# Kernel optimization log

Hardware: AMD Instinct MI355X
Metric: run time of the kernel (lower is better)

Reference implementation:

```python
import jax, jax.numpy as jnp
import numpy as np

B, XL, YL = 4, 128, 1024
D, H, L, DFF = 512, 8, 3, 2048
PV, AV, OV = 512, 1025, 1025
MASK_ID = 1024
EOS = 1024
DUR_W = 1.0
NEG = -1e9  # finite large-negative instead of -inf: keeps fully-padded rows NaN-free
HD = D // H
S = XL + 1 + YL


def sinusoid(n, d):
    pos = jnp.arange(n, dtype=jnp.float32)[:, None]
    div = jnp.exp(jnp.arange(0, d, 2, dtype=jnp.float32) * (-np.log(10000.0) / d))
    pe = jnp.zeros((n, d), dtype=jnp.float32)
    pe = pe.at[:, 0::2].set(jnp.sin(pos * div))
    pe = pe.at[:, 1::2].set(jnp.cos(pos * div))
    return pe


def layer_norm(x, g, b, eps=1e-5):
    mu = x.mean(-1, keepdims=True)
    var = ((x - mu) ** 2).mean(-1, keepdims=True)
    return (x - mu) * jax.lax.rsqrt(var + eps) * g + b


def setup_inputs():
    k = jax.random.split(jax.random.key(0), 32)
    x = jax.random.randint(k[0], (B, XL), 0, PV)
    x1_lens = jax.random.randint(k[1], (B,), 20, 60)
    x2_lens = jax.random.randint(k[2], (B,), 20, 60)
    y = jax.random.randint(k[3], (B, YL), 0, AV - 2)
    y1_lens = jax.random.randint(k[4], (B,), 100, 400)
    y2_lens = jax.random.randint(k[5], (B,), 300, 600)
    y_lens = y1_lens + 1 + y2_lens
    idx = jnp.arange(YL)[None, :]
    valid = (idx >= y1_lens[:, None] + 1) & (idx < y_lens[:, None] - 1)
    bern = jax.random.uniform(k[6], (B, YL)) < 0.3  # mask_ratio = mid(min,max)
    ym = bern & valid
    need = (~ym.any(1)) & valid.any(1)
    first = jnp.argmax(valid, axis=1)
    y_mask = ym | (need[:, None] & (idx == first[:, None]))
    emo_feature = jax.random.normal(k[7], (B, 768), dtype=jnp.float32)

    def n(kk, shape, s=0.02):
        return s * jax.random.normal(kk, shape, dtype=jnp.float32)

    inp = dict(x=x, x1_lens=x1_lens, x2_lens=x2_lens, y=y, y1_lens=y1_lens,
               y2_lens=y2_lens, y_mask=y_mask, emo_feature=emo_feature)
    inp['text_emb'] = n(k[8], (PV, D))
    inp['audio_emb'] = n(k[9], (AV, D))
    inp['type_emb'] = n(k[10], (3, D))
    inp['emo_W'] = n(k[11], (D, 768))
    inp['emo_b'] = jnp.zeros((D,), jnp.float32)
    inp['alpha_text'] = jnp.float32(1.0)
    inp['alpha_audio'] = jnp.float32(1.0)
    inp['Wqkv'] = n(k[12], (L, 3 * D, D))
    inp['bqkv'] = jnp.zeros((L, 3 * D), jnp.float32)
    inp['Wo'] = n(k[13], (L, D, D))
    inp['bo'] = jnp.zeros((L, D), jnp.float32)
    inp['ln1_g'] = jnp.ones((L, D), jnp.float32)
    inp['ln1_b'] = jnp.zeros((L, D), jnp.float32)
    inp['ln2_g'] = jnp.ones((L, D), jnp.float32)
    inp['ln2_b'] = jnp.zeros((L, D), jnp.float32)
    inp['W1'] = n(k[14], (L, DFF, D))
    inp['b1'] = jnp.zeros((L, DFF), jnp.float32)
    inp['W2'] = n(k[15], (L, D, DFF))
    inp['b2'] = jnp.zeros((L, D), jnp.float32)
    inp['predict_W'] = n(k[16], (OV, D))
    inp['dW1'] = n(k[17], (D // 2, D))
    inp['db1'] = jnp.zeros((D // 2,), jnp.float32)
    inp['dW2'] = n(k[18], (D // 4, D // 2))
    inp['db2'] = jnp.zeros((D // 4,), jnp.float32)
    inp['dW3'] = n(k[19], (1, D // 4))
    inp['db3'] = jnp.zeros((1,), jnp.float32)
    return inp


def build_attn_bias(x1_lens, x2_lens, y1_lens, y2_lens, y_mask):
    x_lens = x1_lens + 1 + x2_lens
    y_lens = y1_lens + 1 + y2_lens
    cS = jnp.arange(S)[None, :]  # [1,S] key columns
    # --- x rows ---
    rx = jnp.arange(XL)[None, :]
    is_x1 = rx < x1_lens[:, None]                                   # [B,XL]
    allow_x1 = cS < x1_lens[:, None]                                # [B,S]
    allow_x2 = (cS >= x1_lens[:, None]) & (cS < x_lens[:, None])
    x_allow = jnp.where(is_x1[:, :, None], allow_x1[:, None, :], allow_x2[:, None, :])
    # --- emo row: attends only to itself (col XL) ---
    emo_allow = jnp.broadcast_to((cS == XL)[:, None, :], (B, 1, S))
    # --- y rows ---
    ry = jnp.arange(YL)[None, :]
    is_y1 = ry < y1_lens[:, None]
    is_cls = ry == y1_lens[:, None]
    is_y2 = (ry > y1_lens[:, None]) & (ry < y_lens[:, None])
    allow_y1 = (cS < x1_lens[:, None]) | ((cS > XL) & (cS <= XL + y1_lens[:, None]))
    allow_cls = (cS < x_lens[:, None]) | (cS == XL) | ((cS > XL) & (cS <= XL + y1_lens[:, None] + 1))
    allow_y2 = (cS < x_lens[:, None]) | (cS == XL) | ((cS > XL) & (cS <= XL + y_lens[:, None]))
    ymask_full = jnp.zeros((B, S), bool).at[:, XL + 1:].set(y_mask)
    allow_y2 = allow_y2 & (~ymask_full)                             # masked tokens invisible
    y_allow = jnp.where(is_y1[:, :, None], allow_y1[:, None, :],
               jnp.where(is_cls[:, :, None], allow_cls[:, None, :],
                jnp.where(is_y2[:, :, None], allow_y2[:, None, :], False)))
    block = ~jnp.concatenate([x_allow, emo_allow, y_allow], axis=1)  # True = blocked
    return jnp.where(block, jnp.float32(NEG), jnp.float32(0.0))[:, None]  # [B,1,S,S]


def encoder_forward(h, bias, Wqkv, bqkv, Wo, bo, ln1_g, ln1_b, ln2_g, ln2_b, W1, b1, W2, b2):
    scale = 1.0 / np.sqrt(HD)
    for l in range(L):
        qkv = h @ Wqkv[l].T + bqkv[l]                               # [B,S,3D]
        q, k, v = jnp.split(qkv, 3, axis=-1)
        q = q.reshape(B, S, H, HD).transpose(0, 2, 1, 3)
        k = k.reshape(B, S, H, HD).transpose(0, 2, 1, 3)
        v = v.reshape(B, S, H, HD).transpose(0, 2, 1, 3)
        scores = jnp.einsum('bhqd,bhkd->bhqk', q, k) * scale + bias
        a = jax.nn.softmax(scores, axis=-1)
        o = jnp.einsum('bhqk,bhkd->bhqd', a, v).transpose(0, 2, 1, 3).reshape(B, S, D)
        o = o @ Wo[l].T + bo[l]
        h = layer_norm(h + o, ln1_g[l], ln1_b[l])                   # post-norm
        ff = jax.nn.relu(h @ W1[l].T + b1[l]) @ W2[l].T + b2[l]
        h = layer_norm(h + ff, ln2_g[l], ln2_b[l])
    return h


def reference(x, x1_lens, x2_lens, y, y1_lens, y2_lens, y_mask, emo_feature,
              text_emb, audio_emb, type_emb, emo_W, emo_b, alpha_text, alpha_audio,
              Wqkv, bqkv, Wo, bo, ln1_g, ln1_b, ln2_g, ln2_b, W1, b1, W2, b2,
              predict_W, dW1, db1, dW2, db2, dW3, db3):
    y_target = y
    x_emb = text_emb[x] + type_emb[0]
    x_pos = x_emb + alpha_text * sinusoid(XL, D)
    emo = emo_feature @ emo_W.T + emo_b + type_emb[1]
    y_in = jnp.where(y_mask, MASK_ID, y)
    y_emb = audio_emb[y_in] + type_emb[2]
    y_pos = y_emb + alpha_audio * sinusoid(YL, D)
    h_input = jnp.concatenate([x_pos, emo[:, None, :], y_pos], axis=1)  # [B,S,D]
    bias = build_attn_bias(x1_lens, x2_lens, y1_lens, y2_lens, y_mask)
    enc = encoder_forward(h_input, bias, Wqkv, bqkv, Wo, bo,
                          ln1_g, ln1_b, ln2_g, ln2_b, W1, b1, W2, b2)
    # duration loss on CLS hidden at prompt_lens = XL + 1 + y1_lens
    cls_hidden = enc[jnp.arange(B), XL + 1 + y1_lens]
    h1 = jax.nn.relu(cls_hidden @ dW1.T + db1)
    h2 = jax.nn.relu(h1 @ dW2.T + db2)
    pred_dur = (h2 @ dW3.T + db3)[:, 0]
    tgt_dur = y2_lens.astype(jnp.float32) / x2_lens.astype(jnp.float32)
    e = pred_dur - tgt_dur
    dur_loss = jnp.mean(jnp.where(jnp.abs(e) <= 1.0, 0.5 * e * e, jnp.abs(e) - 0.5))
    # token CE over masked positions (mean over masked tokens)
    logits = enc[:, XL + 1:] @ predict_W.T                          # [B,YL,OV]
    logp = jax.nn.log_softmax(logits, axis=-1)
    ce = -jnp.take_along_axis(logp, y_target[..., None], axis=-1)[..., 0]
    m = y_mask.astype(jnp.float32)
    token_loss = jnp.sum(ce * m) / jnp.sum(m)
    # top-3 accuracy ignoring EOS
    top3 = jax.lax.top_k(logits, 3)[1]
    correct = jnp.any(top3 == y_target[..., None], axis=-1)
    inc = (y_mask & (y_target != EOS)).astype(jnp.float32)
    acc = jnp.sum(correct.astype(jnp.float32) * inc) / jnp.maximum(jnp.sum(inc), 1.0)
    total_loss = token_loss + DUR_W * dur_loss
    return total_loss, acc
```

## Files before the change

kernel.cpp:

```cpp
#include <hip/hip_runtime.h>
#include <hip/hip_bf16.h>
#include <math.h>

#define BATCH 4
#define XL 128
#define YL 1024
#define DMODEL 512
#define NH 8
#define NLAYER 3
#define DFF 2048
#define MASK_ID 1024
#define EOS_TOK 1024
#define HD 64
#define SEQ 1153
#define OV 1025
#define NEGBIG (-1e9f)
#define QBLK 128
#define CCAP 2432

typedef unsigned short u16;
typedef unsigned int u32;
typedef short short8 __attribute__((ext_vector_type(8)));
typedef float f32x4 __attribute__((ext_vector_type(4)));

__device__ __forceinline__ u16 f2bf(float f) {
    union { float f; unsigned u; } v; v.f = f;
    unsigned r = v.u + 0x7fffu + ((v.u >> 16) & 1u);
    return (u16)(r >> 16);
}
__device__ __forceinline__ float bf2f(u16 b) {
    union { unsigned u; float f; } v; v.u = ((unsigned)b) << 16;
    return v.f;
}

__global__ __launch_bounds__(256) void cvt5_kernel(
    const float* __restrict__ s0, u16* __restrict__ d0, int n0,
    const float* __restrict__ s1, u16* __restrict__ d1, int n1,
    const float* __restrict__ s2, u16* __restrict__ d2, int n2,
    const float* __restrict__ s3, u16* __restrict__ d3, int n3,
    const float* __restrict__ s4, u16* __restrict__ d4, int n4)
{
    int c0 = n0, c1 = c0 + n1, c2 = c1 + n2, c3 = c2 + n3, c4 = c3 + n4;
    for (int i = blockIdx.x * 256 + threadIdx.x; i < c4; i += gridDim.x * 256) {
        const float* s; u16* d; int j;
        if (i < c0)      { s = s0; d = d0; j = i; }
        else if (i < c1) { s = s1; d = d1; j = i - c0; }
        else if (i < c2) { s = s2; d = d2; j = i - c1; }
        else if (i < c3) { s = s3; d = d3; j = i - c2; }
        else             { s = s4; d = d4; j = i - c3; }
        float4 v = ((const float4*)s)[j];
        ushort4 o;
        o.x = f2bf(v.x); o.y = f2bf(v.y); o.z = f2bf(v.z); o.w = f2bf(v.w);
        ((ushort4*)d)[j] = o;
    }
}

__global__ __launch_bounds__(256) void emo_kernel(
    const float* __restrict__ emo_feature, const float* __restrict__ emo_W,
    const float* __restrict__ emo_b, const float* __restrict__ type_emb,
    float* __restrict__ hbuf, u16* __restrict__ hbuf_bf)
{
    int b = blockIdx.x >> 3, c = blockIdx.x & 7;
    int t = threadIdx.x;
    int osub = t >> 2, ln = t & 3;
    int d = c * 64 + osub;
    const float* f = emo_feature + b * 768 + ln * 192;
    const float* w = emo_W + (size_t)d * 768 + ln * 192;
    float acc = 0.f;
    #pragma unroll 4
    for (int k = 0; k < 192; ++k) acc = fmaf(f[k], w[k], acc);
    acc += __shfl_xor(acc, 1);
    acc += __shfl_xor(acc, 2);
    if (ln == 0) {
        float v = acc + emo_b[d] + type_emb[DMODEL + d];
        hbuf[(size_t)(b * SEQ + XL) * DMODEL + d] = v;
        hbuf_bf[(size_t)(b * SEQ + XL) * DMODEL + d] = f2bf(v);
    }
}

__global__ __launch_bounds__(256) void build_h_kernel(
    const int* __restrict__ x, const int* __restrict__ y, const int* __restrict__ y_mask,
    const float* __restrict__ text_emb, const float* __restrict__ audio_emb,
    const float* __restrict__ type_emb,
    const float* __restrict__ alpha_text, const float* __restrict__ alpha_audio,
    float* __restrict__ hbuf, u16* __restrict__ hbuf_bf)
{
    int row = blockIdx.x * 4 + (threadIdx.x >> 6);
    int l = threadIdx.x & 63;
    int b = row / SEQ, s = row % SEQ;
    if (s == XL) return;
    int d0 = l * 8;

    const float* emb; const float* te; float alpha; int pos;
    if (s < XL) {
        int tok = x[b * XL + s];
        emb = text_emb + (size_t)tok * DMODEL;
        te = type_emb; alpha = alpha_text[0]; pos = s;
    } else {
        int r = s - XL - 1;
        int tok = y_mask[b * YL + r] ? MASK_ID : y[b * YL + r];
        emb = audio_emb + (size_t)tok * DMODEL;
// ... 156 lines not shown
            #pragma unroll
            for (int jj = 0; jj < 4; ++jj) {
                int row = m0 + wm + i * 16 + ((l >> 4) << 2) + jj;
                int col = n0 + wn + j * 16 + (l & 15);
                if (row < M && col < N)
                    Cp[(size_t)row * N + col] = acc[i][j][jj];
            }
        }
    }
}

__global__ __launch_bounds__(256) void gemm_bf16_splitk_dynm_kernel(
    const u16* __restrict__ A, const u16* __restrict__ Bw,
    const int* __restrict__ Mp,
    float* __restrict__ P0, float* __restrict__ P1,
    int N, int K, int klen)
{
    int M = *Mp;
    int m0 = blockIdx.y * 128;
    if (m0 >= M) return;
    __shared__ u16 As[128 * 32];
    __shared__ u16 Bs[128 * 32];
    int tid = threadIdx.x;
    int w = tid >> 6, l = tid & 63;
    int z = blockIdx.z;
    float* Cp = (z == 0) ? P0 : P1;
    int kbeg = z * klen;
    int kend = min(kbeg + klen, K);
    int n0 = blockIdx.x * 128;
    int wm = (w >> 1) * 64, wn = (w & 1) * 64;

    f32x4 acc[4][4];
    #pragma unroll
    for (int i = 0; i < 4; ++i)
        #pragma unroll
        for (int j = 0; j < 4; ++j) acc[i][j] = (f32x4){0.f, 0.f, 0.f, 0.f};

    int srow0 = (w << 5) + (l >> 2);
    int skp = (l & 3) << 3;

    for (int k0 = kbeg; k0 < kend; k0 += 32) {
        #pragma unroll
        for (int c = 0; c < 2; ++c) {
            int row = srow0 + c * 16;
            int am = m0 + row; if (am >= M) am = M - 1;
            int bn = n0 + row; if (bn >= N) bn = N - 1;
            __builtin_amdgcn_global_load_lds(
                (const __attribute__((address_space(1))) void*)(A + (size_t)am * K + k0 + skp),
                (__attribute__((address_space(3))) void*)(As + ((w * 2 + c) << 9)), 16, 0, 0);
            __builtin_amdgcn_global_load_lds(
                (const __attribute__((address_space(1))) void*)(Bw + (size_t)bn * K + k0 + skp),
                (__attribute__((address_space(3))) void*)(Bs + ((w * 2 + c) << 9)), 16, 0, 0);
        }
        __syncthreads();
        short8 af[4], bfr[4];
        #pragma unroll
        for (int i = 0; i < 4; ++i) {
            af[i]  = *(const short8*)(As + (wm + i * 16 + (l & 15)) * 32 + ((l >> 4) << 3));
            bfr[i] = *(const short8*)(Bs + (wn + i * 16 + (l & 15)) * 32 + ((l >> 4) << 3));
        }
        #pragma unroll
        for (int i = 0; i < 4; ++i)
            #pragma unroll
            for (int j = 0; j < 4; ++j)
                acc[i][j] = __builtin_amdgcn_mfma_f32_16x16x32_bf16(af[i], bfr[j], acc[i][j], 0, 0, 0);
        __syncthreads();
    }

    #pragma unroll
    for (int i = 0; i < 4; ++i) {
        #pragma unroll
        for (int j = 0; j < 4; ++j) {
            #pragma unroll
            for (int jj = 0; jj < 4; ++jj) {
                int row = m0 + wm + i * 16 + ((l >> 4) << 2) + jj;
                int col = n0 + wn + j * 16 + (l & 15);
                if (row < M && col < N)
                    Cp[(size_t)row * N + col] = acc[i][j][jj];
            }
        }
    }
}

__global__ __launch_bounds__(512) void attn_mfma_kernel(
    const u16* __restrict__ qkv,
    const int* __restrict__ x1_lens, const int* __restrict__ x2_lens,
    const int* __restrict__ y1_lens, const int* __restrict__ y2_lens,
    const int* __restrict__ y_mask,
    u16* __restrict__ obuf)
{
    __shared__ u16 Ks[64 * 64];
    __shared__ u16 Vt[64 * 64];
    __shared__ unsigned long long Bits[7][19];

    int tid = threadIdx.x;
    int w = tid >> 6, l = tid & 63;
    int g = l >> 4;
    int bh = blockIdx.y;
    int b = bh >> 3, h = bh & 7;
    int q0 = blockIdx.x * QBLK;

    int x1 = x1_lens[b], xlen = x1 + 1 + x2_lens[b];
    int y1 = y1_lens[b], ylen = y1 + 1 + y2_lens[b];

    int kmax = -1;
    if (q0 < XL) kmax = max(kmax, xlen - 1);
    if (XL >= q0 && XL < q0 + QBLK) kmax = max(kmax, XL);
    {
        int ry0 = max(0, q0 - XL - 1);
        int ry1 = min(YL - 1, q0 + QBLK - 2 - XL);
        if (ry0 <= ry1) {
            if (ry0 <= y1 - 1) kmax = max(kmax, XL + y1);
            if (y1 >= ry0 && y1 <= ry1) kmax = max(kmax, XL + y1 + 1);
            int a = max(ry0, y1 + 1), bb = min(ry1, ylen - 1);
            if (a <= bb) kmax = max(kmax, XL + ylen);
        }
    }
    if (kmax < 0) return;
    int NKT = (kmax >> 6) + 1;

    for (int pp = w; pp < 7 * 19; pp += 8) {
        int ty = pp / 19, tile = pp - ty * 19;
        int c = tile * 64 + l;
        bool allow = false;
        if (c < SEQ && ty < 6) {
            bool a2c = (c == XL), ygt = (c > XL);
            if (ty == 0) allow = (c < x1);
            else if (ty == 1) allow = (c >= x1) && (c < xlen);
            else if (ty == 2) allow = a2c;
            else if (ty == 3) allow = (c < x1) || (ygt && c <= XL + y1);
            else if (ty == 4) allow = (c < xlen) || a2c || (ygt && c <= XL + y1 + 1);
            else {
                int ym = ygt ? y_mask[b * YL + c - XL - 1] : 0;
                allow = (((c < xlen) || a2c || (ygt && c <= XL + ylen)) && !ym);
            }
        }
        unsigned long long mk = __ballot(allow);
        if (l == 0) Bits[ty][tile] = mk;
    }

    int qr = q0 + w * 16 + (l & 15);
    int qrc = min(qr, SEQ - 1);
    short8 qf0, qf1;
    {
        const u16* qp = qkv + (size_t)(b * SEQ + qrc) * 1536 + h * 64 + (g << 3);
        short8 r0 = *(const short8*)qp;
        short8 r1 = *(const short8*)(qp + 32);
        #pragma unroll
        for (int e = 0; e < 8; ++e) {
            qf0[e] = (short)f2bf(bf2f((u16)r0[e]) * 0.125f);
            qf1[e] = (short)f2bf(bf2f((u16)r1[e]) * 0.125f);
        }
    }

    int rt;
    {
        if (qr >= SEQ) rt = 6;
        else if (qr < XL) rt = (qr < x1) ? 0 : 1;
        else if (qr == XL) rt = 2;
        else {
            int ry = qr - XL - 1;
            rt = (ry < y1) ? 3 : (ry == y1) ? 4 : (ry < ylen) ? 5 : 6;
        }
    }

    f32x4 oacc[4];
    #pragma unroll
    for (int db = 0; db < 4; ++db) oacc[db] = (f32x4){0.f, 0.f, 0.f, 0.f};
    float mrun = -INFINITY, lrun = 0.f;

    int srcA = (l & 15) + ((g & 1) << 5);
    int srcB = srcA + 16;
    bool hi = (g >> 1) & 1;

    for (int kt = 0; kt < NKT; ++kt) {
        __syncthreads();
        {
            int r = tid >> 3, d0k = (tid & 7) << 3;
            int krc = min(kt * 64 + r, SEQ - 1);
            short8 ka = *(const short8*)(qkv + (size_t)(b * SEQ + krc) * 1536 + 512 + h * 64 + d0k);
            *(short8*)&Ks[r * 64 + (d0k ^ ((r & 7) << 3))] = ka;
        }
        {
            int rp = tid >> 4, o = tid & 15;
            int d0v = o * 4;
            int k0r = min(kt * 64 + 2 * rp, SEQ - 1);
            int k1r = min(kt * 64 + 2 * rp + 1, SEQ - 1);
            ushort4 va = *(const ushort4*)(qkv + (size_t)(b * SEQ + k0r) * 1536 + 1024 + h * 64 + d0v);
            ushort4 vb = *(const ushort4*)(qkv + (size_t)(b * SEQ + k1r) * 1536 + 1024 + h * 64 + d0v);
            u32 pv[4] = {(u32)va.x | ((u32)vb.x << 16), (u32)va.y | ((u32)vb.y << 16),
                         (u32)va.z | ((u32)vb.z << 16), (u32)va.w | ((u32)vb.w << 16)};
            #pragma unroll
            for (int e = 0; e < 4; ++e) {
                int d = d0v + e;
                *(u32*)&Vt[d * 64 + ((2 * rp) ^ ((d & 7) << 3))] = pv[e];
            }
        }
        __syncthreads();

        f32x4 sc[4];
        #pragma unroll
        for (int cb = 0; cb < 4; ++cb) {
            int krw = cb * 16 + (l & 15);
            int ksw = (krw & 7) << 3;
            short8 k0 = *(const short8*)&Ks[krw * 64 + ((g << 3) ^ ksw)];
            short8 k1 = *(const short8*)&Ks[krw * 64 + ((32 + (g << 3)) ^ ksw)];
            f32x4 z = (f32x4){0.f, 0.f, 0.f, 0.f};
            z = __builtin_amdgcn_mfma_f32_16x16x32_bf16(k0, qf0, z, 0, 0, 0);
            sc[cb] = __builtin_amdgcn_mfma_f32_16x16x32_bf16(k1, qf1, z, 0, 0, 0);
        }

        unsigned long long mb = Bits[rt][kt];
        #pragma unroll
        for (int cb = 0; cb < 4; ++cb) {
            unsigned nib = (unsigned)(mb >> (16 * cb + 4 * g)) & 0xFu;
            #pragma unroll
            for (int r = 0; r < 4; ++r)
                sc[cb][r] = ((nib >> r) & 1u) ? sc[cb][r] : NEGBIG;
        }

        float tmax = sc[0][0];
        #pragma unroll
        for (int cb = 0; cb < 4; ++cb)
            #pragma unroll
            for (int r = 0; r < 4; ++r) tmax = fmaxf(tmax, sc[cb][r]);
        tmax = fmaxf(tmax, __shfl_xor(tmax, 16));
        tmax = fmaxf(tmax, __shfl_xor(tmax, 32));
        float newm = fmaxf(mrun, tmax);
        float corr = __expf(mrun - newm);
        float p[4][4];
        float ps = 0.f;
        #pragma unroll
        for (int cb = 0; cb < 4; ++cb)
            #pragma unroll
            for (int r = 0; r < 4; ++r) {
                p[cb][r] = __expf(sc[cb][r] - newm);
                ps += p[cb][r];
            }
        ps += __shfl_xor(ps, 16);
        ps += __shfl_xor(ps, 32);
        lrun = lrun * corr + ps;
        mrun = newm;

        float cr[4];
        #pragma unroll
        for (int r = 0; r < 4; ++r) cr[r] = __shfl(corr, (g << 2) + r);
        #pragma unroll
        for (int db = 0; db < 4; ++db)
            #pragma unroll
            for (int r = 0; r < 4; ++r) oacc[db][r] *= cr[r];

        u32 P0[4], P1[4];
        #pragma unroll
        for (int cb = 0; cb < 4; ++cb) {
            P0[cb] = (u32)f2bf(p[cb][0]) | ((u32)f2bf(p[cb][1]) << 16);
            P1[cb] = (u32)f2bf(p[cb][2]) | ((u32)f2bf(p[cb][3]) << 16);
        }

        union { u32 u[4]; short8 s; } f1, f2;
        {
            u32 a0 = __shfl(P0[0], srcA), a1 = __shfl(P1[0], srcA);
            u32 a2 = __shfl(P0[0], srcB), a3 = __shfl(P1[0], srcB);
            u32 b0 = __shfl(P0[1], srcA), b1 = __shfl(P1[1], srcA);
            u32 b2 = __shfl(P0[1], srcB), b3 = __shfl(P1[1], srcB);
            f1.u[0] = hi ? b0 : a0; f1.u[1] = hi ? b1 : a1;
            f1.u[2] = hi ? b2 : a2; f1.u[3] = hi ? b3 : a3;
            u32 c0 = __shfl(P0[2], srcA), c1 = __shfl(P1[2], srcA);
            u32 c2 = __shfl(P0[2], srcB), c3 = __shfl(P1[2], srcB);
            u32 d0 = __shfl(P0[3], srcA), d1 = __shfl(P1[3], srcA);
            u32 d2 = __shfl(P0[3], srcB), d3 = __shfl(P1[3], srcB);
            f2.u[0] = hi ? d0 : c0; f2.u[1] = hi ? d1 : c1;
            f2.u[2] = hi ? d2 : c2; f2.u[3] = hi ? d3 : c3;
        }

        #pragma unroll
        for (int db = 0; db < 4; ++db) {
            int vr = db * 16 + (l & 15);
            int vsw = (vr & 7) << 3;
            short8 v0 = *(const short8*)&Vt[vr * 64 + ((g << 3) ^ vsw)];
            short8 v1 = *(const short8*)&Vt[vr * 64 + ((32 + (g << 3)) ^ vsw)];
            oacc[db] = __builtin_amdgcn_mfma_f32_16x16x32_bf16(f1.s, v0, oacc[db], 0, 0, 0);
            oacc[db] = __builtin_amdgcn_mfma_f32_16x16x32_bf16(f2.s, v1, oacc[db], 0, 0, 0);
        }
    }

    float rinv = 1.f / lrun;
    float rl[4];
    #pragma unroll
    for (int r = 0; r < 4; ++r) rl[r] = __shfl(rinv, (g << 2) + r);
    #pragma unroll
    for (int db = 0; db < 4; ++db) {
        #pragma unroll
        for (int r = 0; r < 4; ++r) {
            int qrj = q0 + w * 16 + (g << 2) + r;
            if (qrj < SEQ)
                obuf[(size_t)(b * SEQ + qrj) * DMODEL + h * 64 + db * 16 + (l & 15)] =
                    f2bf(oacc[db][r] * rl[r]);
        }
    }
}

__global__ __launch_bounds__(256) void add_ln_kernel(
    float* __restrict__ hbuf, u16* __restrict__ hbuf_bf,
    const float* __restrict__ p0, const float* __restrict__ p1,
    const float* __restrict__ p2, const float* __restrict__ bias,
    const float* __restrict__ g, const float* __restrict__ beta)
{
    int row = blockIdx.x * 4 + (threadIdx.x >> 6);
    int l = threadIdx.x & 63;
    int d0 = l * 8;
    size_t off = (size_t)row * DMODEL + d0;
    float* hp = hbuf + off;
    float4 a0 = *(const float4*)hp, a1 = *(const float4*)(hp + 4);
    float4 q0 = *(const float4*)(p0 + off), q1 = *(const float4*)(p0 + off + 4);
    float v[8] = {a0.x + q0.x, a0.y + q0.y, a0.z + q0.z, a0.w + q0.w,
                  a1.x + q1.x, a1.y + q1.y, a1.z + q1.z, a1.w + q1.w};
    if (p1) {
        float4 r0 = *(const float4*)(p1 + off), r1 = *(const float4*)(p1 + off + 4);
        v[0] += r0.x; v[1] += r0.y; v[2] += r0.z; v[3] += r0.w;
        v[4] += r1.x; v[5] += r1.y; v[6] += r1.z; v[7] += r1.w;
    }
    if (p2) {
        float4 r0 = *(const float4*)(p2 + off), r1 = *(const float4*)(p2 + off + 4);
        v[0] += r0.x; v[1] += r0.y; v[2] += r0.z; v[3] += r0.w;
        v[4] += r1.x; v[5] += r1.y; v[6] += r1.z; v[7] += r1.w;
    }
    {
        float4 b0 = *(const float4*)(bias + d0), b1 = *(const float4*)(bias + d0 + 4);
        v[0] += b0.x; v[1] += b0.y; v[2] += b0.z; v[3] += b0.w;
        v[4] += b1.x; v[5] += b1.y; v[6] += b1.z; v[7] += b1.w;
    }
    float s = 0.f;
    #pragma unroll
    for (int e = 0; e < 8; ++e) s += v[e];
    #pragma unroll
    for (int off2 = 32; off2 > 0; off2 >>= 1) s += __shfl_xor(s, off2);
    float mu = s * (1.f / DMODEL);
    float sq = 0.f;
    #pragma unroll
    for (int e = 0; e < 8; ++e) { v[e] -= mu; sq += v[e] * v[e]; }
    #pragma unroll
    for (int off2 = 32; off2 > 0; off2 >>= 1) sq += __shfl_xor(sq, off2);
    float inv = 1.f / sqrtf(sq * (1.f / DMODEL) + 1e-5f);
    float4 g0 = *(const float4*)(g + d0), g1 = *(const float4*)(g + d0 + 4);
    float4 be0 = *(const float4*)(beta + d0), be1 = *(const float4*)(beta + d0 + 4);
    float o[8];
    o[0] = v[0] * inv * g0.x + be0.x; o[1] = v[1] * inv * g0.y + be0.y;
    o[2] = v[2] * inv * g0.z + be0.z; o[3] = v[3] * inv * g0.w + be0.w;
    o[4] = v[4] * inv * g1.x + be1.x; o[5] = v[5] * inv * g1.y + be1.y;
    o[6] = v[6] * inv * g1.z + be1.z; o[7] = v[7] * inv * g1.w + be1.w;
    *(float4*)hp       = make_float4(o[0], o[1], o[2], o[3]);
    *(float4*)(hp + 4) = make_float4(o[4], o[5], o[6], o[7]);
    short8 sv;
    #pragma unroll
    for (int e = 0; e < 8; ++e) sv[e] = (short)f2bf(o[e]);
    *(short8*)(hbuf_bf + off) = sv;
}

__global__ __launch_bounds__(256) void init_accum_kernel(float* accum) {
    if (threadIdx.x < 8) accum[threadIdx.x] = 0.f;
}

__global__ __launch_bounds__(256) void compact_kernel(
    const int* __restrict__ y_mask, int* __restrict__ cnt, int* __restrict__ cmap)
{
    int i = blockIdx.x * 256 + threadIdx.x;
    if (i < BATCH * YL && y_mask[i]) {
        int pos = atomicAdd(cnt, 1);
        cmap[pos] = i;
    }
}

__global__ __launch_bounds__(256) void copy_rows_kernel(
    const int* __restrict__ cnt, const int* __restrict__ cmap,
    const u16* __restrict__ hbuf_bf, const int* __restrict__ y,
    u16* __restrict__ cbuf, int* __restrict__ ctgt)
{
    int i = blockIdx.x;
    if (i >= *cnt) return;
    int g = cmap[i];
    int b = g >> 10, r = g & 1023;
    const u16* src = hbuf_bf + (size_t)(b * SEQ + XL + 1 + r) * DMODEL;
// ... 97 lines not shown
        const float* w = dW2 + (size_t)t * 256;
        for (int k = 0; k < 256; ++k) acc = fmaf(h1s[k], w[k], acc);
        h2s[t] = fmaxf(acc, 0.f);
    }
    __syncthreads();
    if (t < 64) {
        float v = h2s[t] * dW3[t] + h2s[t + 64] * dW3[t + 64];
        #pragma unroll
        for (int off = 32; off > 0; off >>= 1) v += __shfl_xor(v, off);
        if (t == 0) preds[b] = v + db3[0];
    }
}

__global__ __launch_bounds__(64) void final_kernel(
    const float* __restrict__ accum, const float* __restrict__ preds,
    const int* __restrict__ y2_lens, const int* __restrict__ x2_lens,
    float* __restrict__ out)
{
    if (threadIdx.x == 0) {
        float dl = 0.f;
        for (int b = 0; b < BATCH; ++b) {
            float tgt = (float)y2_lens[b] / (float)x2_lens[b];
            float e = preds[b] - tgt;
            float ae = fabsf(e);
            dl += (ae <= 1.f) ? 0.5f * e * e : (ae - 0.5f);
        }
        dl *= (1.f / BATCH);
        float token_loss = accum[0] / accum[1];
        float acc_v = accum[2] / fmaxf(accum[3], 1.f);
        out[0] = token_loss + dl;
        out[1] = acc_v;
    }
}

extern "C" void kernel_launch(void* const* d_in, const int* in_sizes, int n_in,
                              void* d_out, int out_size, void* d_ws, size_t ws_size,
                              hipStream_t stream)
{
    const int*   x           = (const int*)d_in[0];
    const int*   x1_lens     = (const int*)d_in[1];
    const int*   x2_lens     = (const int*)d_in[2];
    const int*   y           = (const int*)d_in[3];
    const int*   y1_lens     = (const int*)d_in[4];
    const int*   y2_lens     = (const int*)d_in[5];
    const int*   y_mask      = (const int*)d_in[6];
    const float* emo_feature = (const float*)d_in[7];
    const float* text_emb    = (const float*)d_in[8];
    const float* audio_emb   = (const float*)d_in[9];
    const float* type_emb    = (const float*)d_in[10];
    const float* emo_W       = (const float*)d_in[11];
    const float* emo_b       = (const float*)d_in[12];
    const float* alpha_text  = (const float*)d_in[13];
    const float* alpha_audio = (const float*)d_in[14];
    const float* Wqkv        = (const float*)d_in[15];
    const float* bqkv        = (const float*)d_in[16];
    const float* Wo          = (const float*)d_in[17];
    const float* bo          = (const float*)d_in[18];
    const float* ln1_g       = (const float*)d_in[19];
    const float* ln1_b       = (const float*)d_in[20];
    const float* ln2_g       = (const float*)d_in[21];
    const float* ln2_b       = (const float*)d_in[22];
    const float* W1          = (const float*)d_in[23];
    const float* b1          = (const float*)d_in[24];
    const float* W2          = (const float*)d_in[25];
    const float* b2          = (const float*)d_in[26];
    const float* predict_W   = (const float*)d_in[27];
    const float* dW1         = (const float*)d_in[28];
    const float* db1         = (const float*)d_in[29];
    const float* dW2         = (const float*)d_in[30];
    const float* db2         = (const float*)d_in[31];
    const float* dW3         = (const float*)d_in[32];
    const float* db3         = (const float*)d_in[33];

    const int M = BATCH * SEQ;
    char* p = (char*)d_ws;
    float* hbuf   = (float*)p; p += 9445376;
    float* delta  = (float*)p; p += 9445376;
    char*  uni    = p;         p += 18909440;
    u16*   hbuf_bf = (u16*)p;  p += 4722688;
    u16*   qkv_bf  = (u16*)p;  p += 14168064;
    u16*   obuf_bf = (u16*)p;  p += 4722688;
    u16*   wbf     = (u16*)p;  p += 19923968;
    u16*   cbuf    = (u16*)p;  p += (size_t)CCAP * DMODEL * 2;
    u16*   ff1_bf  = (u16*)uni;

    float* partA = (float*)qkv_bf;
    float* partB = (float*)((char*)qkv_bf + 9445376);
    float* lg0   = (float*)uni;
    float* lg1   = (float*)qkv_bf;

    float* accum  = delta;
    int*   cnt    = (int*)(delta + 4);
    float* preds  = delta + 8;
    int*   cmap   = (int*)(delta + 16);
    int*   ctgt   = cmap + CCAP;
    float* h1buf  = (float*)(ctgt + CCAP);

    u16* wq_bf = wbf;
    u16* wo_bf = wq_bf + 2359296;
    u16* w1_bf = wo_bf + 786432;
    u16* w2_bf = w1_bf + 3145728;
    u16* wp_bf = w2_bf + 3145728;

    cvt5_kernel<<<1024, 256, 0, stream>>>(
        Wqkv, wq_bf, 2359296 / 4,
        Wo, wo_bf, 786432 / 4,
        W1, w1_bf, 3145728 / 4,
        W2, w2_bf, 3145728 / 4,
        predict_W, wp_bf, 524800 / 4);

    emo_kernel<<<32, 256, 0, stream>>>(emo_feature, emo_W, emo_b, type_emb, hbuf, hbuf_bf);
    build_h_kernel<<<M / 4, 256, 0, stream>>>(
        x, y, y_mask, text_emb, audio_emb, type_emb,
        alpha_text, alpha_audio, hbuf, hbuf_bf);

    const int MG = (M + 127) / 128;
    for (int l = 0; l < NLAYER; ++l) {
        gemm_bf16_kernel<<<dim3(12, MG), 256, 0, stream>>>(
            hbuf_bf, wq_bf + (size_t)l * 1536 * 512, bqkv + l * 1536,
            nullptr, qkv_bf, M, 1536, 512, 0);
        attn_mfma_kernel<<<dim3((SEQ + QBLK - 1) / QBLK, BATCH * NH), 512, 0, stream>>>(
            qkv_bf, x1_lens, x2_lens, y1_lens, y2_lens, y_mask, obuf_bf);
        gemm_bf16_splitk_kernel<<<dim3(4, MG, 2), 256, 0, stream>>>(
            obuf_bf, wo_bf + (size_t)l * 512 * 512,
            delta, partA, nullptr, M, 512, 512, 256);
        add_ln_kernel<<<M / 4, 256, 0, stream>>>(hbuf, hbuf_bf,
            delta, partA, nullptr, bo + l * 512,
            ln1_g + l * DMODEL, ln1_b + l * DMODEL);
        gemm_bf16_kernel<<<dim3(16, MG), 256, 0, stream>>>(
            hbuf_bf, w1_bf + (size_t)l * 2048 * 512, b1 + l * 2048,
            nullptr, ff1_bf, M, 2048, 512, 1);
        gemm_bf16_splitk_kernel<<<dim3(4, MG, 3), 256, 0, stream>>>(
            ff1_bf, w2_bf + (size_t)l * 512 * 2048,
            delta, partA, partB, M, 512, 2048, 768);
        add_ln_kernel<<<M / 4, 256, 0, stream>>>(hbuf, hbuf_bf,
            delta, partA, partB, b2 + l * 512,
            ln2_g + l * DMODEL, ln2_b + l * DMODEL);
    }

    init_accum_kernel<<<1, 64, 0, stream>>>(accum);
    compact_kernel<<<(BATCH * YL) / 256, 256, 0, stream>>>(y_mask, cnt, cmap);
    copy_rows_kernel<<<CCAP, 256, 0, stream>>>(cnt, cmap, hbuf_bf, y, cbuf, ctgt);
    gemm_bf16_splitk_dynm_kernel<<<dim3((OV + 127) / 128, CCAP / 128, 2), 256, 0, stream>>>(
        cbuf, wp_bf, cnt, lg0, lg1, OV, 512, 256);
    ce_kernel<<<CCAP, 256, 0, stream>>>(cnt, lg0, lg1, ctgt, accum);

    dur1_kernel<<<32, 256, 0, stream>>>(hbuf, y1_lens, dW1, db1, h1buf);
    dur2_kernel<<<4, 256, 0, stream>>>(h1buf, dW2, db2, dW3, db3, preds);
    final_kernel<<<1, 64, 0, stream>>>(accum, preds, y2_lens, x2_lens, (float*)d_out);
}
```

Before: 598.2 us.

## Double-buffer K/V tiles in attention with register prefetch and MFMA priority

```diff
diff --git a/kernel.cpp b/kernel.cpp
--- a/kernel.cpp
+++ b/kernel.cpp
@@ -346,8 +346,8 @@
     const int* __restrict__ y_mask,
     u16* __restrict__ obuf)
 {
-    __shared__ u16 Ks[64 * 64];
-    __shared__ u16 Vt[64 * 64];
+    __shared__ u16 Ks[2][64 * 64];
+    __shared__ u16 Vt[2][64 * 64];
     __shared__ unsigned long long Bits[7][19];
 
     int tid = threadIdx.x;
@@ -430,42 +430,60 @@
     int srcB = srcA + 16;
     bool hi = (g >> 1) & 1;
 
+    int sr = tid >> 3, sd = (tid & 7) << 3;
+    int ksw_w = (sd ^ ((sr & 7) << 3));
+    int vrp = tid >> 4, vo = (tid & 15) << 2;
+    const u16* kbase = qkv + (size_t)b * SEQ * 1536 + 512 + h * 64;
+    const u16* vbase = kbase + 512;
+
+    short8 kreg; ushort4 va, vb;
+    {
+        int krc = min(sr, SEQ - 1);
+        kreg = *(const short8*)(kbase + (size_t)krc * 1536 + sd);
+        int k0r = min(2 * vrp, SEQ - 1);
+        int k1r = min(2 * vrp + 1, SEQ - 1);
+        va = *(const ushort4*)(vbase + (size_t)k0r * 1536 + vo);
+        vb = *(const ushort4*)(vbase + (size_t)k1r * 1536 + vo);
+    }
+    *(short8*)&Ks[0][sr * 64 + ksw_w] = kreg;
+    {
+        u32 pv[4] = {(u32)va.x | ((u32)vb.x << 16), (u32)va.y | ((u32)vb.y << 16),
+                     (u32)va.z | ((u32)vb.z << 16), (u32)va.w | ((u32)vb.w << 16)};
+        #pragma unroll
+        for (int e = 0; e < 4; ++e) {
+            int d = vo + e;
+            *(u32*)&Vt[0][d * 64 + ((2 * vrp) ^ ((d & 7) << 3))] = pv[e];
+        }
+    }
+
     for (int kt = 0; kt < NKT; ++kt) {
         __syncthreads();
-        {
-            int r = tid >> 3, d0k = (tid & 7) << 3;
-            int krc = min(kt * 64 + r, SEQ - 1);
-            short8 ka = *(const short8*)(qkv + (size_t)(b * SEQ + krc) * 1536 + 512 + h * 64 + d0k);
-            *(short8*)&Ks[r * 64 + (d0k ^ ((r & 7) << 3))] = ka;
-        }
-        {
-            int rp = tid >> 4, o = tid & 15;
-            int d0v = o * 4;
-            int k0r = min(kt * 64 + 2 * rp, SEQ - 1);
-            int k1r = min(kt * 64 + 2 * rp + 1, SEQ - 1);
-            ushort4 va = *(const ushort4*)(qkv + (size_t)(b * SEQ + k0r) * 1536 + 1024 + h * 64 + d0v);
-            ushort4 vb = *(const ushort4*)(qkv + (size_t)(b * SEQ + k1r) * 1536 + 1024 + h * 64 + d0v);
-            u32 pv[4] = {(u32)va.x | ((u32)vb.x << 16), (u32)va.y | ((u32)vb.y << 16),
-                         (u32)va.z | ((u32)vb.z << 16), (u32)va.w | ((u32)vb.w << 16)};
-            #pragma unroll
-            for (int e = 0; e < 4; ++e) {
-                int d = d0v + e;
-                *(u32*)&Vt[d * 64 + ((2 * rp) ^ ((d & 7) << 3))] = pv[e];
-            }
-        }
-        __syncthreads();
+        int cur = kt & 1;
+        bool have_next = (kt + 1 < NKT);
+
+        if (have_next) {
+            int base = (kt + 1) * 64;
+            int krc = min(base + sr, SEQ - 1);
+            kreg = *(const short8*)(kbase + (size_t)krc * 1536 + sd);
+            int k0r = min(base + 2 * vrp, SEQ - 1);
+            int k1r = min(base + 2 * vrp + 1, SEQ - 1);
+            va = *(const ushort4*)(vbase + (size_t)k0r * 1536 + vo);
+            vb = *(const ushort4*)(vbase + (size_t)k1r * 1536 + vo);
+        }
 
         f32x4 sc[4];
+        __builtin_amdgcn_s_setprio(1);
         #pragma unroll
         for (int cb = 0; cb < 4; ++cb) {
             int krw = cb * 16 + (l & 15);
             int ksw = (krw & 7) << 3;
-            short8 k0 = *(const short8*)&Ks[krw * 64 + ((g << 3) ^ ksw)];
-            short8 k1 = *(const short8*)&Ks[krw * 64 + ((32 + (g << 3)) ^ ksw)];
+            short8 k0 = *(const short8*)&Ks[cur][krw * 64 + ((g << 3) ^ ksw)];
+            short8 k1 = *(const short8*)&Ks[cur][krw * 64 + ((32 + (g << 3)) ^ ksw)];
             f32x4 z = (f32x4){0.f, 0.f, 0.f, 0.f};
             z = __builtin_amdgcn_mfma_f32_16x16x32_bf16(k0, qf0, z, 0, 0, 0);
             sc[cb] = __builtin_amdgcn_mfma_f32_16x16x32_bf16(k1, qf1, z, 0, 0, 0);
         }
+        __builtin_amdgcn_s_setprio(0);
 
         unsigned long long mb = Bits[rt][kt];
         #pragma unroll
@@ -530,14 +548,28 @@
             f2.u[2] = hi ? d2 : c2; f2.u[3] = hi ? d3 : c3;
         }
 
+        __builtin_amdgcn_s_setprio(1);
         #pragma unroll
         for (int db = 0; db < 4; ++db) {
             int vr = db * 16 + (l & 15);
             int vsw = (vr & 7) << 3;
-            short8 v0 = *(const short8*)&Vt[vr * 64 + ((g << 3) ^ vsw)];
-            short8 v1 = *(const short8*)&Vt[vr * 64 + ((32 + (g << 3)) ^ vsw)];
+            short8 v0 = *(const short8*)&Vt[cur][vr * 64 + ((g << 3) ^ vsw)];
+            short8 v1 = *(const short8*)&Vt[cur][vr * 64 + ((32 + (g << 3)) ^ vsw)];
             oacc[db] = __builtin_amdgcn_mfma_f32_16x16x32_bf16(f1.s, v0, oacc[db], 0, 0, 0);
             oacc[db] = __builtin_amdgcn_mfma_f32_16x16x32_bf16(f2.s, v1, oacc[db], 0, 0, 0);
+        }
+        __builtin_amdgcn_s_setprio(0);
+
+        if (have_next) {
+            int nxt = cur ^ 1;
+            *(short8*)&Ks[nxt][sr * 64 + ksw_w] = kreg;
+            u32 pv[4] = {(u32)va.x | ((u32)vb.x << 16), (u32)va.y | ((u32)vb.y << 16),
+                         (u32)va.z | ((u32)vb.z << 16), (u32)va.w | ((u32)vb.w << 16)};
+            #pragma unroll
+            for (int e = 0; e < 4; ++e) {
+                int d = vo + e;
+                *(u32*)&Vt[nxt][d * 64 + ((2 * vrp) ^ ((d & 7) << 3))] = pv[e];
+            }
         }
     }
 
```

New measurement: 601.0 us. Within noise of the previous version (+0.5%).

## Pre-transpose V and load K/V fragments directly from global memory in attention

Applied to the files above, without the earlier changes.

```diff
diff --git a/kernel.cpp b/kernel.cpp
--- a/kernel.cpp
+++ b/kernel.cpp
@@ -13,6 +13,7 @@
 #define EOS_TOK 1024
 #define HD 64
 #define SEQ 1153
+#define SEQP 1216
 #define OV 1025
 #define NEGBIG (-1e9f)
 #define QBLK 128
@@ -339,23 +340,53 @@
     }
 }
 
+__global__ __launch_bounds__(256) void vtrans_kernel(
+    const u16* __restrict__ qkv, u16* __restrict__ vt)
+{
+    __shared__ u16 tbuf[64][72];
+    int bh = blockIdx.y;
+    int b = bh >> 3, h = bh & 7;
+    int kt = blockIdx.x;
+    int tid = threadIdx.x;
+    #pragma unroll
+    for (int i = 0; i < 2; ++i) {
+        int idx = tid + i * 256;
+        int r = idx >> 3, d0 = (idx & 7) << 3;
+        int s = kt * 64 + r;
+        short8 v = (short8){0,0,0,0,0,0,0,0};
+        if (s < SEQ)
+            v = *(const short8*)(qkv + (size_t)(b * SEQ + s) * 1536 + 1024 + h * 64 + d0);
+        *(short8*)&tbuf[r][d0] = v;
+    }
+    __syncthreads();
+    u16* out = vt + (size_t)bh * 64 * SEQP + kt * 64;
+    #pragma unroll
+    for (int i = 0; i < 2; ++i) {
+        int idx = tid + i * 256;
+        int d = idx >> 3, s0 = (idx & 7) << 3;
+        short8 v;
+        #pragma unroll
+        for (int e = 0; e < 8; ++e) v[e] = (short)tbuf[s0 + e][d];
+        *(short8*)(out + (size_t)d * SEQP + s0) = v;
+    }
+}
+
 __global__ __launch_bounds__(512) void attn_mfma_kernel(
-    const u16* __restrict__ qkv,
+    const u16* __restrict__ qkv, const u16* __restrict__ vt,
     const int* __restrict__ x1_lens, const int* __restrict__ x2_lens,
     const int* __restrict__ y1_lens, const int* __restrict__ y2_lens,
     const int* __restrict__ y_mask,
     u16* __restrict__ obuf)
 {
-    __shared__ u16 Ks[64 * 64];
-    __shared__ u16 Vt[64 * 64];
     __shared__ unsigned long long Bits[7][19];
 
     int tid = threadIdx.x;
     int w = tid >> 6, l = tid & 63;
     int g = l >> 4;
+    int q = l & 15;
     int bh = blockIdx.y;
     int b = bh >> 3, h = bh & 7;
-    int q0 = blockIdx.x * QBLK;
+    int q0 = (gridDim.x - 1 - blockIdx.x) * QBLK;
 
     int x1 = x1_lens[b], xlen = x1 + 1 + x2_lens[b];
     int y1 = y1_lens[b], ylen = y1 + 1 + y2_lens[b];
@@ -395,8 +426,9 @@
         unsigned long long mk = __ballot(allow);
         if (l == 0) Bits[ty][tile] = mk;
     }
-
-    int qr = q0 + w * 16 + (l & 15);
+    __syncthreads();
+
+    int qr = q0 + w * 16 + q;
     int qrc = min(qr, SEQ - 1);
     short8 qf0, qf1;
     {
@@ -426,46 +458,39 @@
     for (int db = 0; db < 4; ++db) oacc[db] = (f32x4){0.f, 0.f, 0.f, 0.f};
     float mrun = -INFINITY, lrun = 0.f;
 
-    int srcA = (l & 15) + ((g & 1) << 5);
+    int srcA = q + ((g & 1) << 5);
     int srcB = srcA + 16;
     bool hi = (g >> 1) & 1;
 
+    const u16* kbase = qkv + (size_t)b * SEQ * 1536 + 512 + h * 64 + (g << 3);
+    const u16* vbase = vt + (size_t)bh * 64 * SEQP + (size_t)q * SEQP + (g << 3);
+
     for (int kt = 0; kt < NKT; ++kt) {
-        __syncthreads();
-        {
-            int r = tid >> 3, d0k = (tid & 7) << 3;
-            int krc = min(kt * 64 + r, SEQ - 1);
-            short8 ka = *(const short8*)(qkv + (size_t)(b * SEQ + krc) * 1536 + 512 + h * 64 + d0k);
-            *(short8*)&Ks[r * 64 + (d0k ^ ((r & 7) << 3))] = ka;
-        }
-        {
-            int rp = tid >> 4, o = tid & 15;
-            int d0v = o * 4;
-            int k0r = min(kt * 64 + 2 * rp, SEQ - 1);
-            int k1r = min(kt * 64 + 2 * rp + 1, SEQ - 1);
-            ushort4 va = *(const ushort4*)(qkv + (size_t)(b * SEQ + k0r) * 1536 + 1024 + h * 64 + d0v);
-            ushort4 vb = *(const ushort4*)(qkv + (size_t)(b * SEQ + k1r) * 1536 + 1024 + h * 64 + d0v);
-            u32 pv[4] = {(u32)va.x | ((u32)vb.x << 16), (u32)va.y | ((u32)vb.y << 16),
-                         (u32)va.z | ((u32)vb.z << 16), (u32)va.w | ((u32)vb.w << 16)};
-            #pragma unroll
-            for (int e = 0; e < 4; ++e) {
-                int d = d0v + e;
-                *(u32*)&Vt[d * 64 + ((2 * rp) ^ ((d & 7) << 3))] = pv[e];
-            }
-        }
-        __syncthreads();
+        short8 kf0[4], kf1[4];
+        #pragma unroll
+        for (int cb = 0; cb < 4; ++cb) {
+            int ks = min(kt * 64 + cb * 16 + q, SEQ - 1);
+            const u16* kp = kbase + (size_t)ks * 1536;
+            kf0[cb] = *(const short8*)kp;
+            kf1[cb] = *(const short8*)(kp + 32);
+        }
+        short8 vf0[4], vf1[4];
+        #pragma unroll
+        for (int db = 0; db < 4; ++db) {
+            const u16* vp = vbase + (size_t)(db * 16) * SEQP + kt * 64;
+            vf0[db] = *(const short8*)vp;
+            vf1[db] = *(const short8*)(vp + 32);
+        }
 
         f32x4 sc[4];
+        __builtin_amdgcn_s_setprio(1);
         #pragma unroll
         for (int cb = 0; cb < 4; ++cb) {
-            int krw = cb * 16 + (l & 15);
-            int ksw = (krw & 7) << 3;
-            short8 k0 = *(const short8*)&Ks[krw * 64 + ((g << 3) ^ ksw)];
-            short8 k1 = *(const short8*)&Ks[krw * 64 + ((32 + (g << 3)) ^ ksw)];
             f32x4 z = (f32x4){0.f, 0.f, 0.f, 0.f};
-            z = __builtin_amdgcn_mfma_f32_16x16x32_bf16(k0, qf0, z, 0, 0, 0);
-            sc[cb] = __builtin_amdgcn_mfma_f32_16x16x32_bf16(k1, qf1, z, 0, 0, 0);
-        }
+            z = __builtin_amdgcn_mfma_f32_16x16x32_bf16(kf0[cb], qf0, z, 0, 0, 0);
+            sc[cb] = __builtin_amdgcn_mfma_f32_16x16x32_bf16(kf1[cb], qf1, z, 0, 0, 0);
+        }
+        __builtin_amdgcn_s_setprio(0);
 
         unsigned long long mb = Bits[rt][kt];
         #pragma unroll
@@ -530,15 +555,13 @@
             f2.u[2] = hi ? d2 : c2; f2.u[3] = hi ? d3 : c3;
         }
 
+        __builtin_amdgcn_s_setprio(1);
         #pragma unroll
         for (int db = 0; db < 4; ++db) {
-            int vr = db * 16 + (l & 15);
-            int vsw = (vr & 7) << 3;
-            short8 v0 = *(const short8*)&Vt[vr * 64 + ((g << 3) ^ vsw)];
-            short8 v1 = *(const short8*)&Vt[vr * 64 + ((32 + (g << 3)) ^ vsw)];
-            oacc[db] = __builtin_amdgcn_mfma_f32_16x16x32_bf16(f1.s, v0, oacc[db], 0, 0, 0);
-            oacc[db] = __builtin_amdgcn_mfma_f32_16x16x32_bf16(f2.s, v1, oacc[db], 0, 0, 0);
-        }
+            oacc[db] = __builtin_amdgcn_mfma_f32_16x16x32_bf16(f1.s, vf0[db], oacc[db], 0, 0, 0);
+            oacc[db] = __builtin_amdgcn_mfma_f32_16x16x32_bf16(f2.s, vf1[db], oacc[db], 0, 0, 0);
+        }
+        __builtin_amdgcn_s_setprio(0);
     }
 
     float rinv = 1.f / lrun;
@@ -551,7 +574,7 @@
         for (int r = 0; r < 4; ++r) {
             int qrj = q0 + w * 16 + (g << 2) + r;
             if (qrj < SEQ)
-                obuf[(size_t)(b * SEQ + qrj) * DMODEL + h * 64 + db * 16 + (l & 15)] =
+                obuf[(size_t)(b * SEQ + qrj) * DMODEL + h * 64 + db * 16 + q] =
                     f2bf(oacc[db][r] * rl[r]);
         }
     }
@@ -818,6 +841,7 @@
     u16*   obuf_bf = (u16*)p;  p += 4722688;
     u16*   wbf     = (u16*)p;  p += 19923968;
     u16*   cbuf    = (u16*)p;  p += (size_t)CCAP * DMODEL * 2;
+    u16*   vtbuf   = (u16*)p;  p += (size_t)32 * 64 * SEQP * 2;
     u16*   ff1_bf  = (u16*)uni;
 
     float* partA = (float*)qkv_bf;
@@ -855,8 +879,9 @@
         gemm_bf16_kernel<<<dim3(12, MG), 256, 0, stream>>>(
             hbuf_bf, wq_bf + (size_t)l * 1536 * 512, bqkv + l * 1536,
             nullptr, qkv_bf, M, 1536, 512, 0);
+        vtrans_kernel<<<dim3(19, 32), 256, 0, stream>>>(qkv_bf, vtbuf);
         attn_mfma_kernel<<<dim3((SEQ + QBLK - 1) / QBLK, BATCH * NH), 512, 0, stream>>>(
-            qkv_bf, x1_lens, x2_lens, y1_lens, y2_lens, y_mask, obuf_bf);
+            qkv_bf, vtbuf, x1_lens, x2_lens, y1_lens, y2_lens, y_mask, obuf_bf);
         gemm_bf16_splitk_kernel<<<dim3(4, MG, 2), 256, 0, stream>>>(
             obuf_bf, wo_bf + (size_t)l * 512 * 512,
             delta, partA, nullptr, M, 512, 512, 256);
```

After: 726.1 us. 21.4% more time.

## Split attention over key tiles into two halves with a merge kernel

Applied to the files above, without the earlier changes.

```diff
diff --git a/kernel.cpp b/kernel.cpp
--- a/kernel.cpp
+++ b/kernel.cpp
@@ -17,6 +17,7 @@
 #define NEGBIG (-1e9f)
 #define QBLK 128
 #define CCAP 2432
+#define NROWS 36896
 
 typedef unsigned short u16;
 typedef unsigned int u32;
@@ -344,7 +345,7 @@
     const int* __restrict__ x1_lens, const int* __restrict__ x2_lens,
     const int* __restrict__ y1_lens, const int* __restrict__ y2_lens,
     const int* __restrict__ y_mask,
-    u16* __restrict__ obuf)
+    float* __restrict__ opart, float* __restrict__ ml)
 {
     __shared__ u16 Ks[64 * 64];
     __shared__ u16 Vt[64 * 64];
@@ -353,9 +354,11 @@
     int tid = threadIdx.x;
     int w = tid >> 6, l = tid & 63;
     int g = l >> 4;
+    int q = l & 15;
     int bh = blockIdx.y;
     int b = bh >> 3, h = bh & 7;
     int q0 = blockIdx.x * QBLK;
+    int z = blockIdx.z;
 
     int x1 = x1_lens[b], xlen = x1 + 1 + x2_lens[b];
     int y1 = y1_lens[b], ylen = y1 + 1 + y2_lens[b];
@@ -373,8 +376,11 @@
             if (a <= bb) kmax = max(kmax, XL + ylen);
         }
     }
-    if (kmax < 0) return;
+    if (kmax < 0) kmax = 0;
     int NKT = (kmax >> 6) + 1;
+    int half = (NKT + 1) >> 1;
+    int kbeg = z ? half : 0;
+    int kend = z ? NKT : half;
 
     for (int pp = w; pp < 7 * 19; pp += 8) {
         int ty = pp / 19, tile = pp - ty * 19;
@@ -396,7 +402,7 @@
         if (l == 0) Bits[ty][tile] = mk;
     }
 
-    int qr = q0 + w * 16 + (l & 15);
+    int qr = q0 + w * 16 + q;
     int qrc = min(qr, SEQ - 1);
     short8 qf0, qf1;
     {
@@ -426,11 +432,11 @@
     for (int db = 0; db < 4; ++db) oacc[db] = (f32x4){0.f, 0.f, 0.f, 0.f};
     float mrun = -INFINITY, lrun = 0.f;
 
-    int srcA = (l & 15) + ((g & 1) << 5);
+    int srcA = q + ((g & 1) << 5);
     int srcB = srcA + 16;
     bool hi = (g >> 1) & 1;
 
-    for (int kt = 0; kt < NKT; ++kt) {
+    for (int kt = kbeg; kt < kend; ++kt) {
         __syncthreads();
         {
             int r = tid >> 3, d0k = (tid & 7) << 3;
@@ -458,13 +464,13 @@
         f32x4 sc[4];
         #pragma unroll
         for (int cb = 0; cb < 4; ++cb) {
-            int krw = cb * 16 + (l & 15);
+            int krw = cb * 16 + q;
             int ksw = (krw & 7) << 3;
             short8 k0 = *(const short8*)&Ks[krw * 64 + ((g << 3) ^ ksw)];
             short8 k1 = *(const short8*)&Ks[krw * 64 + ((32 + (g << 3)) ^ ksw)];
-            f32x4 z = (f32x4){0.f, 0.f, 0.f, 0.f};
-            z = __builtin_amdgcn_mfma_f32_16x16x32_bf16(k0, qf0, z, 0, 0, 0);
-            sc[cb] = __builtin_amdgcn_mfma_f32_16x16x32_bf16(k1, qf1, z, 0, 0, 0);
+            f32x4 zz = (f32x4){0.f, 0.f, 0.f, 0.f};
+            zz = __builtin_amdgcn_mfma_f32_16x16x32_bf16(k0, qf0, zz, 0, 0, 0);
+            sc[cb] = __builtin_amdgcn_mfma_f32_16x16x32_bf16(k1, qf1, zz, 0, 0, 0);
         }
 
         unsigned long long mb = Bits[rt][kt];
@@ -532,7 +538,7 @@
 
         #pragma unroll
         for (int db = 0; db < 4; ++db) {
-            int vr = db * 16 + (l & 15);
+            int vr = db * 16 + q;
             int vsw = (vr & 7) << 3;
             short8 v0 = *(const short8*)&Vt[vr * 64 + ((g << 3) ^ vsw)];
             short8 v1 = *(const short8*)&Vt[vr * 64 + ((32 + (g << 3)) ^ vsw)];
@@ -541,20 +547,44 @@
         }
     }
 
-    float rinv = 1.f / lrun;
-    float rl[4];
-    #pragma unroll
-    for (int r = 0; r < 4; ++r) rl[r] = __shfl(rinv, (g << 2) + r);
+    if (g == 0) {
+        int row = q0 + w * 16 + q;
+        if (row < SEQ) {
+            int ridx = (b * SEQ + row) * 8 + h;
+            ml[(size_t)(z * 2) * NROWS + ridx] = mrun;
+            ml[(size_t)(z * 2 + 1) * NROWS + ridx] = lrun;
+        }
+    }
+    float* op = opart + (size_t)z * NROWS * 64;
     #pragma unroll
     for (int db = 0; db < 4; ++db) {
         #pragma unroll
         for (int r = 0; r < 4; ++r) {
             int qrj = q0 + w * 16 + (g << 2) + r;
-            if (qrj < SEQ)
-                obuf[(size_t)(b * SEQ + qrj) * DMODEL + h * 64 + db * 16 + (l & 15)] =
-                    f2bf(oacc[db][r] * rl[r]);
-        }
-    }
+            if (qrj < SEQ) {
+                int ridx = (b * SEQ + qrj) * 8 + h;
+                op[(size_t)ridx * 64 + db * 16 + q] = oacc[db][r];
+            }
+        }
+    }
+}
+
+__global__ __launch_bounds__(256) void attn_merge_kernel(
+    const float* __restrict__ opart, const float* __restrict__ ml,
+    u16* __restrict__ obuf)
+{
+    int r = blockIdx.x * 4 + (threadIdx.x >> 6);
+    int d = threadIdx.x & 63;
+    float m0 = ml[r], l0 = ml[NROWS + r];
+    float m1 = ml[2 * NROWS + r], l1 = ml[3 * NROWS + r];
+    float M = fmaxf(m0, m1);
+    float w0 = __expf(m0 - M), w1 = __expf(m1 - M);
+    float denom = w0 * l0 + w1 * l1;
+    float o0 = opart[(size_t)r * 64 + d];
+    float o1 = opart[(size_t)(NROWS + r) * 64 + d];
+    float v = (w0 * o0 + w1 * o1) / denom;
+    int bs = r >> 3, h = r & 7;
+    obuf[(size_t)bs * DMODEL + h * 64 + d] = f2bf(v);
 }
 
 __global__ __launch_bounds__(256) void add_ln_kernel(
@@ -824,6 +854,8 @@
     float* partB = (float*)((char*)qkv_bf + 9445376);
     float* lg0   = (float*)uni;
     float* lg1   = (float*)qkv_bf;
+    float* opart = (float*)uni;
+    float* mlbuf = delta;
 
     float* accum  = delta;
     int*   cnt    = (int*)(delta + 4);
@@ -855,8 +887,9 @@
         gemm_bf16_kernel<<<dim3(12, MG), 256, 0, stream>>>(
             hbuf_bf, wq_bf + (size_t)l * 1536 * 512, bqkv + l * 1536,
             nullptr, qkv_bf, M, 1536, 512, 0);
-        attn_mfma_kernel<<<dim3((SEQ + QBLK - 1) / QBLK, BATCH * NH), 512, 0, stream>>>(
-            qkv_bf, x1_lens, x2_lens, y1_lens, y2_lens, y_mask, obuf_bf);
+        attn_mfma_kernel<<<dim3((SEQ + QBLK - 1) / QBLK, BATCH * NH, 2), 512, 0, stream>>>(
+            qkv_bf, x1_lens, x2_lens, y1_lens, y2_lens, y_mask, opart, mlbuf);
+        attn_merge_kernel<<<NROWS / 4, 256, 0, stream>>>(opart, mlbuf, obuf_bf);
         gemm_bf16_splitk_kernel<<<dim3(4, MG, 2), 256, 0, stream>>>(
             obuf_bf, wo_bf + (size_t)l * 512 * 512,
             delta, partA, nullptr, M, 512, 512, 256);
```

New measurement: 598.5 us. Within noise of the previous version (+0.1%).
